# Performance work log

Hardware: AMD Instinct MI355X
Metric: run time of the kernel (lower is better)

## Reference

```python
import jax, jax.numpy as jnp
import numpy as np

B, C, F_IN, F_OUT = 2048, 63, 250, 250
NEG_SLOPE = 0.2
N = B * C  # flattened node count


def _build_edge_index():
    # fixed fully-connected (no self) graph over the FIRST 63 nodes only
    src = np.array([i for i in range(C) for j in range(C) if i != j], dtype=np.int32)
    dst = np.array([j for i in range(C) for j in range(C) if i != j], dtype=np.int32)
    # PyG GATConv add_self_loops=True: self loop for every node (num_nodes = N)
    loops = np.arange(N, dtype=np.int32)
    src = np.concatenate([src, loops])
    dst = np.concatenate([dst, loops])
    return jnp.asarray(np.stack([src, dst]))  # [2, E]


def setup_inputs() -> dict:
    key = jax.random.key(0)
    kx, kw, ks, kd = jax.random.split(key, 4)
    x = jax.random.normal(kx, (B, 1, C, F_IN), dtype=jnp.float32)
    # GATConv params (heads=1): lin weight, att_src, att_dst, bias
    W = jax.random.normal(kw, (F_IN, F_OUT), dtype=jnp.float32) / np.sqrt(F_IN)
    att_src = jax.random.normal(ks, (F_OUT,), dtype=jnp.float32) / np.sqrt(F_OUT)
    att_dst = jax.random.normal(kd, (F_OUT,), dtype=jnp.float32) / np.sqrt(F_OUT)
    bias = jnp.zeros((F_OUT,), dtype=jnp.float32)
    return {"x": x, "W": W, "att_src": att_src, "att_dst": att_dst,
            "bias": bias, "edge_index": _build_edge_index()}


def reference(x, W, att_src, att_dst, bias, edge_index):
    b, _, c, f = x.shape
    n = b * c
    h = x.reshape(n, f) @ W                      # [N, F_OUT]
    a_src = h @ att_src                          # [N]
    a_dst = h @ att_dst                          # [N]
    src, dst = edge_index[0], edge_index[1]
    e = jax.nn.leaky_relu(a_src[src] + a_dst[dst], NEG_SLOPE)  # [E]
    # segment softmax over incoming edges of each dst node (stable)
    m = jax.ops.segment_max(e, dst, num_segments=n)
    ex = jnp.exp(e - m[dst])
    denom = jax.ops.segment_sum(ex, dst, num_segments=n)
    alpha = ex / denom[dst]                      # [E]
    out = jax.ops.segment_sum(alpha[:, None] * h[src], dst, num_segments=n)
    out = out + bias
    return out.reshape(b, 1, c, -1)              # [B,1,63,F_OUT]
```

## Files before the change

### kernel.cpp

```cpp
#include <hip/hip_runtime.h>
#include <cstdint>
#include <cstddef>

#define M_TOTAL 129024
#define KDIM    250
#define NDIM    250
#define BM      64
#define LASTR   264

typedef float  f32x4  __attribute__((ext_vector_type(4)));
typedef __bf16 bf16x8 __attribute__((ext_vector_type(8)));

static __device__ __forceinline__ unsigned short f2bf(float f) {
  unsigned u = __float_as_uint(f);
  u += 0x7fffu + ((u >> 16) & 1u);
  return (unsigned short)(u >> 16);
}

static __device__ __forceinline__ float wsum(float v) {
#pragma unroll
  for (int o = 32; o > 0; o >>= 1) v += __shfl_xor(v, o, 64);
  return v;
}
static __device__ __forceinline__ float wmaxr(float v) {
#pragma unroll
  for (int o = 32; o > 0; o >>= 1) v = fmaxf(v, __shfl_xor(v, o, 64));
  return v;
}

__global__ void wcvt_kernel(const float* __restrict__ W, unsigned short* __restrict__ WTf) {
  const int f     = blockIdx.x * 256 + threadIdx.x;
  const int lane  = f & 63;
  const int kk    = (f >> 6) & 7;
  const int ntile = f >> 9;
  const int n     = ntile * 16 + (lane & 15);
  const int k0    = kk * 32 + (lane >> 4) * 8;
  unsigned u[4];
#pragma unroll
  for (int p = 0; p < 4; ++p) {
    const int ka = k0 + 2 * p, kb = k0 + 2 * p + 1;
    unsigned short a = (n < NDIM && ka < KDIM) ? f2bf(W[(size_t)ka * NDIM + n]) : 0;
    unsigned short b = (n < NDIM && kb < KDIM) ? f2bf(W[(size_t)kb * NDIM + n]) : 0;
    u[p] = (unsigned)a | ((unsigned)b << 16);
  }
  *reinterpret_cast<uint4*>(WTf + (size_t)f * 8) = make_uint4(u[0], u[1], u[2], u[3]);
}

__global__ __launch_bounds__(256, 2) void gemm_kernel(
    const float* __restrict__ X, const unsigned short* __restrict__ WTf,
    const float* __restrict__ bias, float* __restrict__ out,
    float* __restrict__ h63) {
  __shared__ unsigned short lA[BM * LASTR];

  const int mBase = blockIdx.x * BM;
  const int tid  = threadIdx.x;
  const int lane = tid & 63;
  const int w    = tid >> 6;
  const int r16  = lane & 15;
  const int quad = lane >> 4;

  const float* Xs = X + (size_t)mBase * KDIM;

  float2 av[32];
#pragma unroll
  for (int j = 0; j < 32; ++j) {
    const int idx = j * 256 + tid;
    if (j < 31 || tid < 64)
      av[j] = *reinterpret_cast<const float2*>(Xs + (size_t)idx * 2);
  }

  bf16x8 bfrag[4][8];
#pragma unroll
  for (int nt = 0; nt < 4; ++nt)
#pragma unroll
    for (int kk = 0; kk < 8; ++kk)
      bfrag[nt][kk] = *reinterpret_cast<const bf16x8*>(
          WTf + (size_t)((((w * 4 + nt) * 8) + kk) * 64 + lane) * 8);

#pragma unroll
  for (int j = 0; j < 32; ++j) {
    const int idx = j * 256 + tid;
    if (j < 31 || tid < 64) {
      const int r = idx / 125;
      const int c = idx - r * 125;
      const unsigned p = (unsigned)f2bf(av[j].x) | ((unsigned)f2bf(av[j].y) << 16);
      *reinterpret_cast<unsigned*>(&lA[r * LASTR + c * 2]) = p;
    }
  }
  if (tid < 64) {
#pragma unroll
    for (int c = 250; c < 264; c += 2)
      *reinterpret_cast<unsigned*>(&lA[tid * LASTR + c]) = 0u;
  }
  __syncthreads();

  f32x4 acc[4][4];
#pragma unroll
  for (int mt = 0; mt < 4; ++mt)
#pragma unroll
    for (int nt = 0; nt < 4; ++nt)
      acc[mt][nt] = f32x4{0.f, 0.f, 0.f, 0.f};

#pragma unroll
  for (int kk = 0; kk < 8; ++kk) {
    bf16x8 aF[4];
#pragma unroll
    for (int mt = 0; mt < 4; ++mt)
      aF[mt] = *reinterpret_cast<const bf16x8*>(
          &lA[(mt * 16 + r16) * LASTR + kk * 32 + quad * 8]);
#pragma unroll
    for (int mt = 0; mt < 4; ++mt)
#pragma unroll
      for (int nt = 0; nt < 4; ++nt)
        acc[mt][nt] = __builtin_amdgcn_mfma_f32_16x16x32_bf16(aF[mt], bfrag[nt][kk],
                                                              acc[mt][nt], 0, 0, 0);
  }

#pragma unroll
  for (int nt = 0; nt < 4; ++nt) {
    const int col = w * 64 + nt * 16 + r16;
    if (col < NDIM) {
      const float bv = bias[col];
#pragma unroll
      for (int mt = 0; mt < 4; ++mt) {
        const int rb = mBase + mt * 16 + quad * 4;
        f32x4 a = acc[mt][nt];
#pragma unroll
        for (int i = 0; i < 4; ++i)
          out[(size_t)(rb + i) * NDIM + col] = a[i] + bv;
      }
    }
  }
  if (mBase == 0) {
#pragma unroll
    for (int nt = 0; nt < 4; ++nt) {
      const int col = w * 64 + nt * 16 + r16;
      if (col < NDIM) {
#pragma unroll
        for (int mt = 0; mt < 4; ++mt) {
          const int rb = mt * 16 + quad * 4;
          f32x4 a = acc[mt][nt];
#pragma unroll
          for (int i = 0; i < 4; ++i)
            if (rb + i < 63) h63[(rb + i) * NDIM + col] = a[i];
        }
      }
    }
  }
}

__global__ void att_kernel(const float* __restrict__ h, const float* __restrict__ att_src,
                           const float* __restrict__ att_dst, const float* __restrict__ bias,
                           float* __restrict__ out) {
  const int d = blockIdx.x;
  const int tid = threadIdx.x;
  const int lane = tid & 63;
  const int wid = tid >> 6;

  __shared__ float s_asrc[64];
  __shared__ float s_adst;
  __shared__ float s_alpha[64];

  for (int s = wid; s < 63; s += 4) {
    float sum = 0.f;
    for (int f = lane; f < NDIM; f += 64) sum += h[s * NDIM + f] * att_src[f];
    sum = wsum(sum);
    if (lane == 0) s_asrc[s] = sum;
  }
  if (wid == 0) {
    float sum = 0.f;
    for (int f = lane; f < NDIM; f += 64) sum += h[d * NDIM + f] * att_dst[f];
    sum = wsum(sum);
    if (lane == 0) s_adst = sum;
  }
  __syncthreads();

  if (wid == 0) {
    float e = -__builtin_inff();
    if (lane < 63) {
      float x = s_asrc[lane] + s_adst;
      e = (x > 0.f) ? x : 0.2f * x;
    }
    const float m = wmaxr(e);
    const float p = (lane < 63) ? expf(e - m) : 0.f;
    const float den = wsum(p);
    s_alpha[lane] = p / den;
  }
  __syncthreads();

  const int f = tid;
  if (f < NDIM) {
    float o = bias[f];
    for (int s = 0; s < 63; ++s) o += s_alpha[s] * h[s * NDIM + f];
    out[(size_t)d * NDIM + f] = o;
  }
}

extern "C" void kernel_launch(void* const* d_in, const int* in_sizes, int n_in,
                              void* d_out, int out_size, void* d_ws, size_t ws_size,
                              hipStream_t stream) {
  const float* X       = (const float*)d_in[0];
  const float* W       = (const float*)d_in[1];
  const float* att_src = (const float*)d_in[2];
  const float* att_dst = (const float*)d_in[3];
  const float* bias    = (const float*)d_in[4];
  float* out = (float*)d_out;

  unsigned short* WTf = (unsigned short*)d_ws;
  float* h63 = (float*)((char*)d_ws + 131072);

  wcvt_kernel<<<32, 256, 0, stream>>>(W, WTf);
  gemm_kernel<<<M_TOTAL / BM, 256, 0, stream>>>(X, WTf, bias, out, h63);
  att_kernel<<<63, 256, 0, stream>>>(h63, att_src, att_dst, bias, out);
}
```

Measured before the change: 284.5 us.

## Make GEMM persistent with double-buffered direct global-to-LDS loads of X tiles

The GEMM kernel becomes persistent: each of 504 blocks processes 8 tiles of 32 rows. X tiles are streamed as fp32 straight into LDS with global_load_lds into two buffers, so the next tile's load overlaps the current tile's MFMA work. W fragments and bias are loaded once per block. The MFMA operands are swapped so W acts as the A operand and X rows as B, which lets output be written as float2 stores. This removes per-block register staging and repeated W loads. In exchange, the bf16 conversion now happens on every LDS read, and fp32 tiles double the LDS footprint.

```diff
diff --git a/kernel.cpp b/kernel.cpp
--- a/kernel.cpp
+++ b/kernel.cpp
@@ -5,10 +5,14 @@
 #define M_TOTAL 129024
 #define KDIM    250
 #define NDIM    250
-#define BM      64
-#define LASTR   264
+#define BM      32
+#define TPB     8
+#define NBLK    504
+#define TILE_F  (BM*KDIM)
+#define LDSF    8008
 
 typedef float  f32x4  __attribute__((ext_vector_type(4)));
+typedef float  f32x2  __attribute__((ext_vector_type(2)));
 typedef __bf16 bf16x8 __attribute__((ext_vector_type(8)));
 
 static __device__ __forceinline__ unsigned short f2bf(float f) {
@@ -26,6 +30,17 @@
 #pragma unroll
   for (int o = 32; o > 0; o >>= 1) v = fmaxf(v, __shfl_xor(v, o, 64));
   return v;
+}
+
+static __device__ __forceinline__ void gll16(const float* g, float* l) {
+  __builtin_amdgcn_global_load_lds(
+      (const __attribute__((address_space(1))) void*)g,
+      (__attribute__((address_space(3))) void*)l, 16, 0, 0);
+}
+static __device__ __forceinline__ void gll4(const float* g, float* l) {
+  __builtin_amdgcn_global_load_lds(
+      (const __attribute__((address_space(1))) void*)g,
+      (__attribute__((address_space(3))) void*)l, 4, 0, 0);
 }
 
 __global__ void wcvt_kernel(const float* __restrict__ W, unsigned short* __restrict__ WTf) {
@@ -50,99 +65,125 @@
     const float* __restrict__ X, const unsigned short* __restrict__ WTf,
     const float* __restrict__ bias, float* __restrict__ out,
     float* __restrict__ h63) {
-  __shared__ unsigned short lA[BM * LASTR];
-
-  const int mBase = blockIdx.x * BM;
+  __shared__ __attribute__((aligned(16))) float lX[2 * LDSF];
+
   const int tid  = threadIdx.x;
   const int lane = tid & 63;
   const int w    = tid >> 6;
   const int r16  = lane & 15;
   const int quad = lane >> 4;
 
-  const float* Xs = X + (size_t)mBase * KDIM;
-
-  float2 av[32];
-#pragma unroll
-  for (int j = 0; j < 32; ++j) {
-    const int idx = j * 256 + tid;
-    if (j < 31 || tid < 64)
-      av[j] = *reinterpret_cast<const float2*>(Xs + (size_t)idx * 2);
-  }
-
-  bf16x8 bfrag[4][8];
-#pragma unroll
-  for (int nt = 0; nt < 4; ++nt)
+  if (tid < 8) { lX[TILE_F + tid] = 0.f; lX[LDSF + TILE_F + tid] = 0.f; }
+
+  bf16x8 wf[4][8];
+#pragma unroll
+  for (int ft = 0; ft < 4; ++ft)
 #pragma unroll
     for (int kk = 0; kk < 8; ++kk)
-      bfrag[nt][kk] = *reinterpret_cast<const bf16x8*>(
-          WTf + (size_t)((((w * 4 + nt) * 8) + kk) * 64 + lane) * 8);
-
-#pragma unroll
-  for (int j = 0; j < 32; ++j) {
-    const int idx = j * 256 + tid;
-    if (j < 31 || tid < 64) {
-      const int r = idx / 125;
-      const int c = idx - r * 125;
-      const unsigned p = (unsigned)f2bf(av[j].x) | ((unsigned)f2bf(av[j].y) << 16);
-      *reinterpret_cast<unsigned*>(&lA[r * LASTR + c * 2]) = p;
-    }
-  }
-  if (tid < 64) {
-#pragma unroll
-    for (int c = 250; c < 264; c += 2)
-      *reinterpret_cast<unsigned*>(&lA[tid * LASTR + c]) = 0u;
-  }
-  __syncthreads();
-
-  f32x4 acc[4][4];
-#pragma unroll
-  for (int mt = 0; mt < 4; ++mt)
-#pragma unroll
-    for (int nt = 0; nt < 4; ++nt)
-      acc[mt][nt] = f32x4{0.f, 0.f, 0.f, 0.f};
-
-#pragma unroll
-  for (int kk = 0; kk < 8; ++kk) {
-    bf16x8 aF[4];
-#pragma unroll
-    for (int mt = 0; mt < 4; ++mt)
-      aF[mt] = *reinterpret_cast<const bf16x8*>(
-          &lA[(mt * 16 + r16) * LASTR + kk * 32 + quad * 8]);
-#pragma unroll
-    for (int mt = 0; mt < 4; ++mt)
-#pragma unroll
-      for (int nt = 0; nt < 4; ++nt)
-        acc[mt][nt] = __builtin_amdgcn_mfma_f32_16x16x32_bf16(aF[mt], bfrag[nt][kk],
-                                                              acc[mt][nt], 0, 0, 0);
-  }
-
-#pragma unroll
-  for (int nt = 0; nt < 4; ++nt) {
-    const int col = w * 64 + nt * 16 + r16;
-    if (col < NDIM) {
-      const float bv = bias[col];
-#pragma unroll
-      for (int mt = 0; mt < 4; ++mt) {
-        const int rb = mBase + mt * 16 + quad * 4;
-        f32x4 a = acc[mt][nt];
-#pragma unroll
-        for (int i = 0; i < 4; ++i)
-          out[(size_t)(rb + i) * NDIM + col] = a[i] + bv;
-      }
-    }
-  }
-  if (mBase == 0) {
-#pragma unroll
-    for (int nt = 0; nt < 4; ++nt) {
-      const int col = w * 64 + nt * 16 + r16;
-      if (col < NDIM) {
-#pragma unroll
-        for (int mt = 0; mt < 4; ++mt) {
-          const int rb = mt * 16 + quad * 4;
-          f32x4 a = acc[mt][nt];
-#pragma unroll
-          for (int i = 0; i < 4; ++i)
-            if (rb + i < 63) h63[(rb + i) * NDIM + col] = a[i];
+      wf[ft][kk] = *reinterpret_cast<const bf16x8*>(
+          WTf + (size_t)((((w * 4 + ft) * 8) + kk) * 64 + lane) * 8);
+
+  float bv[4][4];
+#pragma unroll
+  for (int ft = 0; ft < 4; ++ft)
+#pragma unroll
+    for (int i = 0; i < 4; ++i) {
+      const int c = w * 64 + ft * 16 + quad * 4 + i;
+      bv[ft][i] = (c < NDIM) ? bias[c] : 0.f;
+    }
+
+  const int tile0 = blockIdx.x * TPB;
+
+  auto stage = [&](int buf, int g) {
+    const float* gb = X + (size_t)g * TILE_F;
+    float* lb = &lX[buf * LDSF];
+    if (w < 3) {
+#pragma unroll
+      for (int c = 0; c < 8; ++c) {
+        const int ch = w * 8 + c;
+        gll16(gb + ch * 256 + lane * 4, lb + ch * 256);
+      }
+    } else {
+#pragma unroll
+      for (int c = 0; c < 7; ++c) {
+        const int ch = 24 + c;
+        gll16(gb + ch * 256 + lane * 4, lb + ch * 256);
+      }
+      gll4(gb + 7936 + lane, lb + 7936);
+    }
+  };
+
+  stage(0, tile0);
+
+  for (int t = 0; t < TPB; ++t) {
+    const int cur = t & 1;
+    __syncthreads();
+    if (t + 1 < TPB) stage(cur ^ 1, tile0 + t + 1);
+
+    const float* Bp = &lX[cur * LDSF];
+    f32x4 acc[4][2];
+#pragma unroll
+    for (int ft = 0; ft < 4; ++ft)
+#pragma unroll
+      for (int nt = 0; nt < 2; ++nt) acc[ft][nt] = f32x4{0.f, 0.f, 0.f, 0.f};
+
+#pragma unroll
+    for (int kk = 0; kk < 8; ++kk) {
+      bf16x8 xf[2];
+#pragma unroll
+      for (int nt = 0; nt < 2; ++nt) {
+        const float* p = Bp + (size_t)(nt * 16 + r16) * KDIM + kk * 32 + quad * 8;
+        const f32x2 a = *reinterpret_cast<const f32x2*>(p);
+        const f32x2 b = *reinterpret_cast<const f32x2*>(p + 2);
+        const f32x2 c = *reinterpret_cast<const f32x2*>(p + 4);
+        const f32x2 d = *reinterpret_cast<const f32x2*>(p + 6);
+        bf16x8 v;
+        v[0] = (__bf16)a.x; v[1] = (__bf16)a.y;
+        v[2] = (__bf16)b.x; v[3] = (__bf16)b.y;
+        v[4] = (__bf16)c.x; v[5] = (__bf16)c.y;
+        v[6] = (__bf16)d.x; v[7] = (__bf16)d.y;
+        xf[nt] = v;
+      }
+#pragma unroll
+      for (int ft = 0; ft < 4; ++ft)
+#pragma unroll
+        for (int nt = 0; nt < 2; ++nt)
+          acc[ft][nt] = __builtin_amdgcn_mfma_f32_16x16x32_bf16(
+              wf[ft][kk], xf[nt], acc[ft][nt], 0, 0, 0);
+    }
+
+    const int rbase = (tile0 + t) * BM;
+#pragma unroll
+    for (int ft = 0; ft < 4; ++ft) {
+      const int c0 = w * 64 + ft * 16 + quad * 4;
+#pragma unroll
+      for (int nt = 0; nt < 2; ++nt) {
+        const int row = rbase + nt * 16 + r16;
+        float* o = out + (size_t)row * NDIM + c0;
+        const f32x4 a = acc[ft][nt];
+        if (c0 + 1 < NDIM) {
+          f32x2 s = {a.x + bv[ft][0], a.y + bv[ft][1]};
+          *reinterpret_cast<f32x2*>(o) = s;
+        }
+        if (c0 + 3 < NDIM) {
+          f32x2 s = {a.z + bv[ft][2], a.w + bv[ft][3]};
+          *reinterpret_cast<f32x2*>(o + 2) = s;
+        }
+      }
+    }
+    if (rbase < 63) {
+#pragma unroll
+      for (int ft = 0; ft < 4; ++ft) {
+        const int c0 = w * 64 + ft * 16 + quad * 4;
+#pragma unroll
+        for (int nt = 0; nt < 2; ++nt) {
+          const int row = rbase + nt * 16 + r16;
+          if (row < 63) {
+            const f32x4 a = acc[ft][nt];
+#pragma unroll
+            for (int i = 0; i < 4; ++i)
+              if (c0 + i < NDIM) h63[(size_t)row * NDIM + c0 + i] = a[i];
+          }
         }
       }
     }
@@ -210,6 +251,6 @@
   float* h63 = (float*)((char*)d_ws + 131072);
 
   wcvt_kernel<<<32, 256, 0, stream>>>(W, WTf);
-  gemm_kernel<<<M_TOTAL / BM, 256, 0, stream>>>(X, WTf, bias, out, h63);
+  gemm_kernel<<<NBLK, 256, 0, stream>>>(X, WTf, bias, out, h63);
   att_kernel<<<63, 256, 0, stream>>>(h63, att_src, att_dst, bias, out);
 }
```

New measurement: 283.2 us. No clear change (-0.4%).

## Compute transposed GEMM tiles per wave without LDS staging

Applied to the files above, without the earlier changes.

The GEMM no longer stages the bf16 A tile in shared memory. Each wave now owns 16 rows and computes the whole transposed output (W^T·X^T), loading X directly from global memory into the MFMA B operand and streaming W fragments from global or L2 on every k-step. This removes the LDS round-trip and the block barrier, and lets each lane write contiguous output columns as float2 stores. The cost is far more global reads of W per wave, since each wave rereads the whole weight instead of holding a quarter of it in registers. Occupancy is raised to three blocks per SM.

```diff
diff --git a/kernel.cpp b/kernel.cpp
--- a/kernel.cpp
+++ b/kernel.cpp
@@ -5,10 +5,11 @@
 #define M_TOTAL 129024
 #define KDIM    250
 #define NDIM    250
-#define BM      64
-#define LASTR   264
+#define NTILES  (M_TOTAL / 16)
+#define NBLK    (NTILES / 4)
 
 typedef float  f32x4  __attribute__((ext_vector_type(4)));
+typedef float  f32x2  __attribute__((ext_vector_type(2)));
 typedef __bf16 bf16x8 __attribute__((ext_vector_type(8)));
 
 static __device__ __forceinline__ unsigned short f2bf(float f) {
@@ -46,103 +47,84 @@
   *reinterpret_cast<uint4*>(WTf + (size_t)f * 8) = make_uint4(u[0], u[1], u[2], u[3]);
 }
 
-__global__ __launch_bounds__(256, 2) void gemm_kernel(
+__global__ __launch_bounds__(256, 3) void gemm_kernel(
     const float* __restrict__ X, const unsigned short* __restrict__ WTf,
     const float* __restrict__ bias, float* __restrict__ out,
     float* __restrict__ h63) {
-  __shared__ unsigned short lA[BM * LASTR];
-
-  const int mBase = blockIdx.x * BM;
   const int tid  = threadIdx.x;
   const int lane = tid & 63;
   const int w    = tid >> 6;
   const int r16  = lane & 15;
   const int quad = lane >> 4;
 
-  const float* Xs = X + (size_t)mBase * KDIM;
+  const int gid = blockIdx.x * 4 + w;
+  const int row = gid * 16 + r16;
+  const float* Xr = X + (size_t)row * KDIM;
 
-  float2 av[32];
+  f32x4 acc[16];
 #pragma unroll
-  for (int j = 0; j < 32; ++j) {
-    const int idx = j * 256 + tid;
-    if (j < 31 || tid < 64)
-      av[j] = *reinterpret_cast<const float2*>(Xs + (size_t)idx * 2);
-  }
-
-  bf16x8 bfrag[4][8];
-#pragma unroll
-  for (int nt = 0; nt < 4; ++nt)
-#pragma unroll
-    for (int kk = 0; kk < 8; ++kk)
-      bfrag[nt][kk] = *reinterpret_cast<const bf16x8*>(
-          WTf + (size_t)((((w * 4 + nt) * 8) + kk) * 64 + lane) * 8);
-
-#pragma unroll
-  for (int j = 0; j < 32; ++j) {
-    const int idx = j * 256 + tid;
-    if (j < 31 || tid < 64) {
-      const int r = idx / 125;
-      const int c = idx - r * 125;
-      const unsigned p = (unsigned)f2bf(av[j].x) | ((unsigned)f2bf(av[j].y) << 16);
-      *reinterpret_cast<unsigned*>(&lA[r * LASTR + c * 2]) = p;
-    }
-  }
-  if (tid < 64) {
-#pragma unroll
-    for (int c = 250; c < 264; c += 2)
-      *reinterpret_cast<unsigned*>(&lA[tid * LASTR + c]) = 0u;
-  }
-  __syncthreads();
-
-  f32x4 acc[4][4];
-#pragma unroll
-  for (int mt = 0; mt < 4; ++mt)
-#pragma unroll
-    for (int nt = 0; nt < 4; ++nt)
-      acc[mt][nt] = f32x4{0.f, 0.f, 0.f, 0.f};
+  for (int ft = 0; ft < 16; ++ft) acc[ft] = f32x4{0.f, 0.f, 0.f, 0.f};
 
 #pragma unroll
   for (int kk = 0; kk < 8; ++kk) {
-    bf16x8 aF[4];
+    const int k0 = kk * 32 + quad * 8;
+    f32x2 xa, xb, xc, xd;
+    if (kk < 7) {
+      xa = *reinterpret_cast<const f32x2*>(Xr + k0);
+      xb = *reinterpret_cast<const f32x2*>(Xr + k0 + 2);
+      xc = *reinterpret_cast<const f32x2*>(Xr + k0 + 4);
+      xd = *reinterpret_cast<const f32x2*>(Xr + k0 + 6);
+    } else {
+      xa = *reinterpret_cast<const f32x2*>(Xr + k0);
+      if (quad < 3) {
+        xb = *reinterpret_cast<const f32x2*>(Xr + k0 + 2);
+        xc = *reinterpret_cast<const f32x2*>(Xr + k0 + 4);
+        xd = *reinterpret_cast<const f32x2*>(Xr + k0 + 6);
+      } else {
+        xb = f32x2{0.f, 0.f}; xc = f32x2{0.f, 0.f}; xd = f32x2{0.f, 0.f};
+      }
+    }
+    bf16x8 xf;
+    xf[0] = (__bf16)xa.x; xf[1] = (__bf16)xa.y;
+    xf[2] = (__bf16)xb.x; xf[3] = (__bf16)xb.y;
+    xf[4] = (__bf16)xc.x; xf[5] = (__bf16)xc.y;
+    xf[6] = (__bf16)xd.x; xf[7] = (__bf16)xd.y;
+
+    const unsigned short* wp = WTf + (size_t)(kk * 64 + lane) * 8;
 #pragma unroll
-    for (int mt = 0; mt < 4; ++mt)
-      aF[mt] = *reinterpret_cast<const bf16x8*>(
-          &lA[(mt * 16 + r16) * LASTR + kk * 32 + quad * 8]);
-#pragma unroll
-    for (int mt = 0; mt < 4; ++mt)
-#pragma unroll
-      for (int nt = 0; nt < 4; ++nt)
-        acc[mt][nt] = __builtin_amdgcn_mfma_f32_16x16x32_bf16(aF[mt], bfrag[nt][kk],
-                                                              acc[mt][nt], 0, 0, 0);
+    for (int ft = 0; ft < 16; ++ft) {
+      const bf16x8 wf = *reinterpret_cast<const bf16x8*>(wp + (size_t)ft * (8 * 64 * 8));
+      acc[ft] = __builtin_amdgcn_mfma_f32_16x16x32_bf16(wf, xf, acc[ft], 0, 0, 0);
+    }
   }
 
+  float* orow = out + (size_t)row * NDIM;
 #pragma unroll
-  for (int nt = 0; nt < 4; ++nt) {
-    const int col = w * 64 + nt * 16 + r16;
-    if (col < NDIM) {
-      const float bv = bias[col];
-#pragma unroll
-      for (int mt = 0; mt < 4; ++mt) {
-        const int rb = mBase + mt * 16 + quad * 4;
-        f32x4 a = acc[mt][nt];
-#pragma unroll
-        for (int i = 0; i < 4; ++i)
-          out[(size_t)(rb + i) * NDIM + col] = a[i] + bv;
-      }
+  for (int ft = 0; ft < 16; ++ft) {
+    const int c0 = ft * 16 + quad * 4;
+    const f32x4 a = acc[ft];
+    if (c0 + 3 < NDIM) {
+      const f32x4 bb = *reinterpret_cast<const f32x4*>(bias + c0);
+      *reinterpret_cast<f32x2*>(orow + c0)     = f32x2{a.x + bb.x, a.y + bb.y};
+      *reinterpret_cast<f32x2*>(orow + c0 + 2) = f32x2{a.z + bb.z, a.w + bb.w};
+    } else if (c0 + 1 < NDIM) {
+      const f32x2 bb = *reinterpret_cast<const f32x2*>(bias + c0);
+      *reinterpret_cast<f32x2*>(orow + c0) = f32x2{a.x + bb.x, a.y + bb.y};
     }
   }
-  if (mBase == 0) {
+
+  if (gid < 4) {
+    if (row < 63) {
+      float* hp = h63 + (size_t)row * NDIM;
 #pragma unroll
-    for (int nt = 0; nt < 4; ++nt) {
-      const int col = w * 64 + nt * 16 + r16;
-      if (col < NDIM) {
-#pragma unroll
-        for (int mt = 0; mt < 4; ++mt) {
-          const int rb = mt * 16 + quad * 4;
-          f32x4 a = acc[mt][nt];
-#pragma unroll
-          for (int i = 0; i < 4; ++i)
-            if (rb + i < 63) h63[(rb + i) * NDIM + col] = a[i];
+      for (int ft = 0; ft < 16; ++ft) {
+        const int c0 = ft * 16 + quad * 4;
+        const f32x4 a = acc[ft];
+        if (c0 + 3 < NDIM) {
+          *reinterpret_cast<f32x2*>(hp + c0)     = f32x2{a.x, a.y};
+          *reinterpret_cast<f32x2*>(hp + c0 + 2) = f32x2{a.z, a.w};
+        } else if (c0 + 1 < NDIM) {
+          *reinterpret_cast<f32x2*>(hp + c0) = f32x2{a.x, a.y};
         }
       }
     }
@@ -210,6 +192,6 @@
   float* h63 = (float*)((char*)d_ws + 131072);
 
   wcvt_kernel<<<32, 256, 0, stream>>>(W, WTf);
-  gemm_kernel<<<M_TOTAL / BM, 256, 0, stream>>>(X, WTf, bias, out, h63);
+  gemm_kernel<<<NBLK, 256, 0, stream>>>(X, WTf, bias, out, h63);
   att_kernel<<<63, 256, 0, stream>>>(h63, att_src, att_dst, bias, out);
 }
```

Result: slower. 333.1 us (+17.1%).
